# Optimization experiments

Hardware: AMD Instinct MI355X
Metric: run time of the kernel (lower is better)

The kernel has to match this reference:

```python
import jax, jax.numpy as jnp
import numpy as np


def setup_inputs() -> dict:
    key = jax.random.key(0)
    k1, k2, k3, k4 = jax.random.split(key, 4)
    B, T, M = 4, 2048, 1024   # batch, seq, d_model -> S = 8192 tokens
    E, F = 16, 4096           # experts (world_size*num_local_experts), d_ff
    x = jax.random.normal(k1, (B, T, M), dtype=jnp.float32) * 0.02
    Wg = jax.random.normal(k2, (M, E), dtype=jnp.float32) * 0.02
    w1 = jax.random.normal(k3, (E, M, F), dtype=jnp.float32) * 0.02
    w2 = jax.random.normal(k4, (E, F, M), dtype=jnp.float32) * 0.02
    return {"x": x, "Wg": Wg, "w1": w1, "w2": w2}


def reference(x, Wg, w1, w2):
    d = x.shape[-1]
    xr = x.reshape(-1, d)                     # (S, M)
    S = xr.shape[0]
    E = Wg.shape[1]
    C = (S + E - 1) // E                      # capacity (capacity_factor = 1.0)

    # top-1 gating (gate module = linear + softmax)
    gate = jax.nn.softmax(xr @ Wg, axis=-1)   # (S, E)
    idx = jnp.argmax(gate, axis=1)            # (S,) expert index per token
    gates_s = jnp.take_along_axis(gate, idx[:, None], axis=1)[:, 0]  # (S,)

    # cumulative-sum location within chosen expert
    onehot = jax.nn.one_hot(idx, E, dtype=jnp.int32)           # (S, E)
    loc = jnp.sum((jnp.cumsum(onehot, axis=0) - 1) * onehot, axis=1)  # (S,)
    valid = loc < C                                             # capacity drop mask

    # scatter dispatch: overflow tokens routed to a pad slot C, then sliced off
    loc_pad = jnp.minimum(loc, C)
    dispatched = jnp.zeros((E, C + 1, d), dtype=x.dtype).at[idx, loc_pad].set(xr)
    dispatched = dispatched[:, :C]            # (E, C, M)

    # all-to-all is identity (FakeAllToAllOp); per-expert FFN
    h = jax.nn.relu(jnp.einsum('ecm,emf->ecf', dispatched, w1))   # (E, C, F)
    expert_out = jnp.einsum('ecf,efm->ecm', h, w2)                # (E, C, M)

    # gather combine: rout[i] = gate_s[i] * expert_out[idx[i], loc[i]] if loc < C
    gathered = expert_out[idx, jnp.minimum(loc, C - 1)]           # (S, M)
    combined = gathered * (gates_s * valid.astype(x.dtype))[:, None]
    return combined.reshape(x.shape)
```

## Files before the change

kernel.cpp:

```cpp
#include <hip/hip_runtime.h>
#include <cstdint>
#include <cstddef>

#define S_TOK 8192
#define DM    1024
#define NE    16
#define NF    4096
#define CAP   512

typedef __attribute__((ext_vector_type(8))) short bf16x8;
typedef __attribute__((ext_vector_type(4))) float f32x4;

__device__ __forceinline__ unsigned short f2bf(float f) {
  __bf16 b = (__bf16)f;
  return __builtin_bit_cast(unsigned short, b);
}
__device__ __forceinline__ unsigned pk2(float a, float b) {
  return (unsigned)f2bf(a) | ((unsigned)f2bf(b) << 16);
}
__device__ __forceinline__ int pcol(int c) { return c ^ ((c >> 3) & 7); }

__device__ __forceinline__ void gload_lds16(const void* g, void* l) {
  __builtin_amdgcn_global_load_lds(
      (const __attribute__((address_space(1))) void*)g,
      (__attribute__((address_space(3))) void*)l, 16, 0, 0);
}

__global__ void __launch_bounds__(256)
cvt_kernel(const float* __restrict__ X, unsigned short* __restrict__ Xb) {
  const int t = blockIdx.x * 256 + threadIdx.x;
  const float4* src = (const float4*)X + (size_t)t * 4;
  float4 v0 = src[0], v1 = src[1], v2 = src[2], v3 = src[3];
  uint4 o0 = make_uint4(pk2(v0.x, v0.y), pk2(v0.z, v0.w),
                        pk2(v1.x, v1.y), pk2(v1.z, v1.w));
  uint4 o1 = make_uint4(pk2(v2.x, v2.y), pk2(v2.z, v2.w),
                        pk2(v3.x, v3.y), pk2(v3.z, v3.w));
  uint4* dst = (uint4*)Xb + (size_t)t * 2;
  dst[0] = o0; dst[1] = o1;
}

__global__ void __launch_bounds__(256)
gate_kernel(const float* __restrict__ X, const float* __restrict__ Wg,
            int* __restrict__ idx, float* __restrict__ gval) {
  const int tid  = threadIdx.x;
  const int lane = tid & 63;
  const int wid  = tid >> 6;
  const int e = lane & 15, q = lane >> 4;
  const int t0 = blockIdx.x * 16 + wid * 4;
  const int mbase = q * 256;

  const float* xp0 = X + (size_t)(t0 + 0) * DM + mbase;
  const float* xp1 = X + (size_t)(t0 + 1) * DM + mbase;
  const float* xp2 = X + (size_t)(t0 + 2) * DM + mbase;
  const float* xp3 = X + (size_t)(t0 + 3) * DM + mbase;
  const float* wp  = Wg + (size_t)mbase * NE + e;

  float a0 = 0.f, a1 = 0.f, a2 = 0.f, a3 = 0.f;
#pragma unroll 4
  for (int i = 0; i < 64; ++i) {
    float4 x0 = *(const float4*)(xp0 + i * 4);
    float4 x1 = *(const float4*)(xp1 + i * 4);
    float4 x2 = *(const float4*)(xp2 + i * 4);
    float4 x3 = *(const float4*)(xp3 + i * 4);
    float w0 = wp[(i * 4 + 0) * NE];
    float w1 = wp[(i * 4 + 1) * NE];
    float w2 = wp[(i * 4 + 2) * NE];
    float w3 = wp[(i * 4 + 3) * NE];
    a0 = fmaf(x0.x, w0, fmaf(x0.y, w1, fmaf(x0.z, w2, fmaf(x0.w, w3, a0))));
    a1 = fmaf(x1.x, w0, fmaf(x1.y, w1, fmaf(x1.z, w2, fmaf(x1.w, w3, a1))));
    a2 = fmaf(x2.x, w0, fmaf(x2.y, w1, fmaf(x2.z, w2, fmaf(x2.w, w3, a2))));
    a3 = fmaf(x3.x, w0, fmaf(x3.y, w1, fmaf(x3.z, w2, fmaf(x3.w, w3, a3))));
  }
#pragma unroll
  for (int s = 16; s < 64; s <<= 1) {
    a0 += __shfl_xor(a0, s, 64);
    a1 += __shfl_xor(a1, s, 64);
    a2 += __shfl_xor(a2, s, 64);
    a3 += __shfl_xor(a3, s, 64);
  }
  float l = (q == 0) ? a0 : (q == 1) ? a1 : (q == 2) ? a2 : a3;
  float bv = l; int bi = e;
#pragma unroll
  for (int s = 1; s < 16; s <<= 1) {
    float ov = __shfl_xor(bv, s, 16);
    int   oi = __shfl_xor(bi, s, 16);
    if (ov > bv || (ov == bv && oi < bi)) { bv = ov; bi = oi; }
  }
  float p  = expf(l - bv);
  float sm = p;
#pragma unroll
  for (int s = 1; s < 16; s <<= 1) sm += __shfl_xor(sm, s, 16);
  if (e == 0) {
    idx[t0 + q]  = bi;
    gval[t0 + q] = 1.0f / sm;
  }
}

__global__ void __launch_bounds__(1024)
scan_kernel(const int* __restrict__ idx, int* __restrict__ s2t) {
  const int tid = threadIdx.x;
#pragma unroll
  for (int k = 0; k < 8; ++k) s2t[tid + k * 1024] = -1;
  __shared__ int base[16];
  __shared__ int wavecnt[16][16];
  if (tid < 16) base[tid] = 0;
  __syncthreads();
  const int wid = tid >> 6, lane = tid & 63;
  const unsigned long long ltmask = (1ull << lane) - 1ull;
  for (int c = 0; c < 8; ++c) {
    const int t = c * 1024 + tid;
    const int e = idx[t];
    int rank = 0;
#pragma unroll
    for (int ee = 0; ee < 16; ++ee) {
      unsigned long long m = __ballot(e == ee);
      if (lane == 0) wavecnt[wid][ee] = __popcll(m);
      if (ee == e) rank = __popcll(m & ltmask);
    }
    __syncthreads();
    if (tid < 16) {
      int s = base[tid];
#pragma unroll
      for (int w = 0; w < 16; ++w) { int cc = wavecnt[w][tid]; wavecnt[w][tid] = s; s += cc; }
      base[tid] = s;
    }
    __syncthreads();
    const int loc = wavecnt[wid][e] + rank;
    if (loc < CAP) s2t[e * CAP + loc] = t;
    __syncthreads();
  }
}



#define G1_BX 2
#define G1_BY 32
#define G1_BZ 16
__global__ void __launch_bounds__(512, 2)
gemm1_kernel(const unsigned short* __restrict__ Xb, const float* __restrict__ W1,
             const int* __restrict__ s2t, unsigned short* __restrict__ H2) {
  constexpr int NT = DM / 64;
  __shared__ __align__(16) char lds[131072];

  const int tid = threadIdx.x;
  const int lane = tid & 63, wid = tid >> 6;
  const int wr = wid >> 1, wc = wid & 1;
  const int ln15 = lane & 15, l16 = lane >> 4;

  int flat = blockIdx.x + G1_BX * (blockIdx.y + G1_BY * blockIdx.z);
  flat = (flat & 7) * (G1_BX * G1_BY * G1_BZ / 8) + (flat >> 3);
  const int bx = flat % G1_BX;
  const int by = (flat / G1_BX) % G1_BY;
  const int e  = flat / (G1_BX * G1_BY);
  const int m0 = bx * 256, n0 = by * 128;

  char* const Bb0 = lds + 98304;
  char* const Bb1 = lds + 98304 + 16384;

  const int rb = wid >> 1;
  const int tok = s2t[e * CAP + m0 + rb * 64 + lane];
  const char* const asrc = (const char*)Xb + (size_t)(tok < 0 ? 0 : tok) * 2048;
  const int kgw = (wid & 1) * 4;
  const int adst = kgw * 4096 + rb * 1024;

  const int c0 = (tid & 31) * 4;
  const int kq = tid >> 5;
  const float* const bsrc = W1 + (size_t)e * DM * NF + (size_t)(kq * 4) * NF + n0 + c0;
  const int kgb = kq >> 1, hb = kq & 1;
  int bwoff[4];
#pragma unroll
  for (int cc = 0; cc < 4; ++cc) bwoff[cc] = kgb * 2048 + pcol(c0 + cc) * 16 + hb * 8;

  int aoff[4], boff[4];
#pragma unroll
  for (int mi = 0; mi < 4; ++mi) aoff[mi] = l16 * 4096 + (wr * 64 + mi * 16 + ln15) * 16;
#pragma unroll
  for (int ni = 0; ni < 4; ++ni) boff[ni] = l16 * 2048 + pcol(wc * 64 + ni * 16 + ln15) * 16;

  f32x4 acc[4][4];
#pragma unroll
  for (int mi = 0; mi < 4; ++mi)
#pragma unroll
    for (int ni = 0; ni < 4; ++ni) acc[mi][ni] = f32x4{0.f, 0.f, 0.f, 0.f};

  float4 breg[4];

  auto ISSUE_B = [&](int kt) {
    const float* bp = bsrc + (size_t)kt * 64 * NF;
#pragma unroll
    for (int r = 0; r < 4; ++r) breg[r] = *(const float4*)(bp + (size_t)r * NF);
  };
  auto ISSUE_A = [&](int Aoff, int kt) {
#pragma unroll
    for (int j = 0; j < 4; ++j)
      gload_lds16(asrc + kt * 128 + (kgw + j) * 16, lds + Aoff + adst + j * 4096);
  };
  auto WRITEB = [&](char* Bbuf) {
    const float* f = (const float*)breg;
#pragma unroll
    for (int cc = 0; cc < 4; ++cc)
      *(uint2*)(Bbuf + bwoff[cc]) =
          make_uint2(pk2(f[0 + cc], f[4 + cc]), pk2(f[8 + cc], f[12 + cc]));
  };
  auto COMPUTE = [&](int Aoff, const char* Bbuf) {
#pragma unroll
    for (int kk = 0; kk < 2; ++kk) {
      bf16x8 af[4], bf[4];
#pragma unroll
      for (int mi = 0; mi < 4; ++mi)
        af[mi] = *(const bf16x8*)(lds + Aoff + kk * 16384 + aoff[mi]);
#pragma unroll
      for (int ni = 0; ni < 4; ++ni)
        bf[ni] = *(const bf16x8*)(Bbuf + kk * 8192 + boff[ni]);
#pragma unroll
      for (int mi = 0; mi < 4; ++mi)
#pragma unroll
        for (int ni = 0; ni < 4; ++ni)
          acc[mi][ni] = __builtin_amdgcn_mfma_f32_16x16x32_bf16(af[mi], bf[ni], acc[mi][ni], 0, 0, 0);
    }
  };

  ISSUE_B(0); ISSUE_A(0, 0);
  WRITEB(Bb0);
  ISSUE_B(1); ISSUE_A(32768, 1);
  asm volatile("s_waitcnt vmcnt(8) lgkmcnt(0)" ::: "memory");
  __builtin_amdgcn_s_barrier();

  int aCur = 0, aNxt = 32768, aNx2 = 65536;
  for (int kt = 0; kt < NT; ++kt) {
    WRITEB((kt & 1) ? Bb0 : Bb1);
    const int tl = (kt + 2 < NT) ? kt + 2 : NT - 1;
    ISSUE_B(tl);
    ISSUE_A(aNx2, tl);
    COMPUTE(aCur, (kt & 1) ? Bb1 : Bb0);
    asm volatile("s_waitcnt vmcnt(8) lgkmcnt(0)" ::: "memory");
    __builtin_amdgcn_s_barrier();
    const int t = aCur; aCur = aNxt; aNxt = aNx2; aNx2 = t;
  }
  asm volatile("s_waitcnt vmcnt(0)" ::: "memory");
  __builtin_amdgcn_s_barrier();

  char* img = lds;
#pragma unroll
  for (int mi = 0; mi < 4; ++mi) {
#pragma unroll
    for (int ni = 0; ni < 4; ++ni) {
      const int colL = wc * 64 + ni * 16 + ln15;
      const int basei = (colL >> 6) * 32768 + ((colL >> 3) & 7) * 4096 + (colL & 7) * 2;
#pragma unroll
      for (int j = 0; j < 4; ++j) {
        const int rowL = wr * 64 + mi * 16 + l16 * 4 + j;
        float v = acc[mi][ni][j];
        v = v > 0.f ? v : 0.f;
        *(unsigned short*)(img + basei + rowL * 16) = f2bf(v);
      }
    }
  }
  __syncthreads();
  const char* src = img + tid * 128;
  char* dst = (char*)H2 + (size_t)e * 4194304 +
              (size_t)((n0 >> 6) + (tid >> 8)) * 65536 +
              (size_t)((tid >> 5) & 7) * 8192 +
              (size_t)(m0 + (tid & 31) * 8) * 16;
#pragma unroll
  for (int u = 0; u < 8; ++u)
    *(uint4*)(dst + u * 16) = *(const uint4*)(src + u * 16);
}

#define G2_BX 2
#define G2_BY 8
#define G2_BZ 16
__global__ void __launch_bounds__(512, 2)
gemm2_kernel(const unsigned short* __restrict__ H2, const float* __restrict__ W2,
             const int* __restrict__ s2t, const float* __restrict__ gval,
             float* __restrict__ Out) {
  constexpr int NT = NF / 64;
  __shared__ __align__(16) char lds[131072];

  const int tid = threadIdx.x;
  const int lane = tid & 63, wid = tid >> 6;
  const int wr = wid >> 1, wc = wid & 1;
  const int ln15 = lane & 15, l16 = lane >> 4;

  int flat = blockIdx.x + G2_BX * (blockIdx.y + G2_BY * blockIdx.z);
  flat = (flat & 7) * (G2_BX * G2_BY * G2_BZ / 8) + (flat >> 3);
  const int bx = flat % G2_BX;
  const int by = (flat / G2_BX) % G2_BY;
  const int e  = flat / (G2_BX * G2_BY);
  const int m0 = bx * 256, n0 = by * 128;

  char* const Bb0 = lds + 98304;
  char* const Bb1 = lds + 98304 + 16384;

  const int rb = wid >> 1;
  const int kgw = (wid & 1) * 4;
  const int adst = kgw * 4096 + rb * 1024;
  const char* const Hex = (const char*)H2 + (size_t)e * 4194304 + (size_t)m0 * 16 +
                          (size_t)(rb * 64 + lane) * 16;

  const int c0 = (tid & 31) * 4;
  const int kq = tid >> 5;
  const float* const bsrc = W2 + (size_t)e * NF * DM + (size_t)(kq * 4) * DM + n0 + c0;
  const int kgb = kq >> 1, hb = kq & 1;
  int bwoff[4];
#pragma unroll
  for (int cc = 0; cc < 4; ++cc) bwoff[cc] = kgb * 2048 + pcol(c0 + cc) * 16 + hb * 8;

  int aoff[4], boff[4];
#pragma unroll
  for (int mi = 0; mi < 4; ++mi) aoff[mi] = l16 * 4096 + (wr * 64 + mi * 16 + ln15) * 16;
#pragma unroll
  for (int ni = 0; ni < 4; ++ni) boff[ni] = l16 * 2048 + pcol(wc * 64 + ni * 16 + ln15) * 16;

  f32x4 acc[4][4];
#pragma unroll
  for (int mi = 0; mi < 4; ++mi)
#pragma unroll
    for (int ni = 0; ni < 4; ++ni) acc[mi][ni] = f32x4{0.f, 0.f, 0.f, 0.f};

  float4 breg[4];

  auto ISSUE_B = [&](int kt) {
    const float* bp = bsrc + (size_t)kt * 64 * DM;
#pragma unroll
    for (int r = 0; r < 4; ++r) breg[r] = *(const float4*)(bp + (size_t)r * DM);
  };
  auto ISSUE_A = [&](int Aoff, int kt) {
#pragma unroll
    for (int j = 0; j < 4; ++j)
      gload_lds16(Hex + (size_t)kt * 65536 + (size_t)(kgw + j) * 8192,
                  lds + Aoff + adst + j * 4096);
  };
  auto WRITEB = [&](char* Bbuf) {
    const float* f = (const float*)breg;
#pragma unroll
    for (int cc = 0; cc < 4; ++cc)
      *(uint2*)(Bbuf + bwoff[cc]) =
          make_uint2(pk2(f[0 + cc], f[4 + cc]), pk2(f[8 + cc], f[12 + cc]));
  };
  auto COMPUTE = [&](int Aoff, const char* Bbuf) {
#pragma unroll
    for (int kk = 0; kk < 2; ++kk) {
      bf16x8 af[4], bf[4];
#pragma unroll
      for (int mi = 0; mi < 4; ++mi)
        af[mi] = *(const bf16x8*)(lds + Aoff + kk * 16384 + aoff[mi]);
#pragma unroll
      for (int ni = 0; ni < 4; ++ni)
        bf[ni] = *(const bf16x8*)(Bbuf + kk * 8192 + boff[ni]);
#pragma unroll
      for (int mi = 0; mi < 4; ++mi)
#pragma unroll
        for (int ni = 0; ni < 4; ++ni)
          acc[mi][ni] = __builtin_amdgcn_mfma_f32_16x16x32_bf16(af[mi], bf[ni], acc[mi][ni], 0, 0, 0);
    }
  };

  ISSUE_B(0); ISSUE_A(0, 0);
  WRITEB(Bb0);
  ISSUE_B(1); ISSUE_A(32768, 1);
  asm volatile("s_waitcnt vmcnt(8) lgkmcnt(0)" ::: "memory");
  __builtin_amdgcn_s_barrier();

  int aCur = 0, aNxt = 32768, aNx2 = 65536;
  for (int kt = 0; kt < NT; ++kt) {
    WRITEB((kt & 1) ? Bb0 : Bb1);
    const int tl = (kt + 2 < NT) ? kt + 2 : NT - 1;
    ISSUE_B(tl);
    ISSUE_A(aNx2, tl);
    COMPUTE(aCur, (kt & 1) ? Bb1 : Bb0);
    asm volatile("s_waitcnt vmcnt(8) lgkmcnt(0)" ::: "memory");
    __builtin_amdgcn_s_barrier();
    const int t = aCur; aCur = aNxt; aNxt = aNx2; aNx2 = t;
  }
  asm volatile("s_waitcnt vmcnt(0)" ::: "memory");

#pragma unroll
  for (int mi = 0; mi < 4; ++mi) {
#pragma unroll
    for (int ni = 0; ni < 4; ++ni) {
      const int col = n0 + wc * 64 + ni * 16 + ln15;
#pragma unroll
      for (int j = 0; j < 4; ++j) {
        const int row = m0 + wr * 64 + mi * 16 + l16 * 4 + j;
        const int tk = s2t[e * CAP + row];
        if (tk >= 0)
          Out[(size_t)tk * DM + col] = acc[mi][ni][j] * gval[tk];
      }
    }
  }
}

extern "C" void kernel_launch(void* const* d_in, const int* in_sizes, int n_in,
                              void* d_out, int out_size, void* d_ws, size_t ws_size,
                              hipStream_t stream) {
  (void)in_sizes; (void)n_in; (void)ws_size;
  const float* X  = (const float*)d_in[0];
  const float* Wg = (const float*)d_in[1];
  const float* W1 = (const float*)d_in[2];
  const float* W2 = (const float*)d_in[3];
  float* Out = (float*)d_out;

  char* ws = (char*)d_ws;
  int*   s2t  = (int*)ws;
  int*   idx  = (int*)(ws + 32768);
  float* gval = (float*)(ws + 65536);
  unsigned short* Xb = (unsigned short*)(ws + 98304);
  unsigned short* H2 = (unsigned short*)(ws + 98304 + 16777216);

  (void)hipMemsetAsync(d_out, 0, (size_t)out_size * sizeof(float), stream);
  cvt_kernel<<<2048, 256, 0, stream>>>(X, Xb);
  gate_kernel<<<S_TOK / 16, 256, 0, stream>>>(X, Wg, idx, gval);
  scan_kernel<<<1, 1024, 0, stream>>>(idx, s2t);
  gemm1_kernel<<<dim3(G1_BX, G1_BY, G1_BZ), 512, 0, stream>>>(Xb, W1, s2t, H2);
  gemm2_kernel<<<dim3(G2_BX, G2_BY, G2_BZ), 512, 0, stream>>>(H2, W2, s2t, gval, Out);
}
```

Measured before the change: 305.2 us.

## Replace bf16 convert with gather into k-major dispatched layout; remap XCD blocks

Drops the whole-tensor bf16 conversion and instead gathers only the dispatched tokens after the scan, converting to bf16 and writing them in a k-group-major per-expert layout. gemm1 then loads A tiles with contiguous, coalesced 16-byte loads and no longer does a per-lane token indirection. Block-to-expert mapping is also changed so each XCD handles two whole experts, aiming for better L2 reuse of expert weights. The gather now runs after the scan on the critical path instead of in parallel with gating, and it zero-fills empty slots.

Measured after the change: 280.7 us. 1.09x faster.

```diff
diff --git a/kernel.cpp b/kernel.cpp
--- a/kernel.cpp
+++ b/kernel.cpp
@@ -24,19 +24,6 @@
   __builtin_amdgcn_global_load_lds(
       (const __attribute__((address_space(1))) void*)g,
       (__attribute__((address_space(3))) void*)l, 16, 0, 0);
-}
-
-__global__ void __launch_bounds__(256)
-cvt_kernel(const float* __restrict__ X, unsigned short* __restrict__ Xb) {
-  const int t = blockIdx.x * 256 + threadIdx.x;
-  const float4* src = (const float4*)X + (size_t)t * 4;
-  float4 v0 = src[0], v1 = src[1], v2 = src[2], v3 = src[3];
-  uint4 o0 = make_uint4(pk2(v0.x, v0.y), pk2(v0.z, v0.w),
-                        pk2(v1.x, v1.y), pk2(v1.z, v1.w));
-  uint4 o1 = make_uint4(pk2(v2.x, v2.y), pk2(v2.z, v2.w),
-                        pk2(v3.x, v3.y), pk2(v3.z, v3.w));
-  uint4* dst = (uint4*)Xb + (size_t)t * 2;
-  dst[0] = o0; dst[1] = o1;
 }
 
 __global__ void __launch_bounds__(256)
@@ -131,14 +118,42 @@
   }
 }
 
+__global__ void __launch_bounds__(256)
+gather_kernel(const float* __restrict__ X, const int* __restrict__ s2t,
+              unsigned short* __restrict__ Xg) {
+  const int tid = threadIdx.x;
+  const int d  = tid & 127;
+  const int sl = tid >> 7;
+  const int s0 = blockIdx.x * 16;
+#pragma unroll 2
+  for (int p = 0; p < 8; ++p) {
+    const int s = s0 + p * 2 + sl;
+    const int tok = s2t[s];
+    uint4 w;
+    if (tok >= 0) {
+      const float* xp = X + (size_t)tok * DM + d * 8;
+      float4 v0 = *(const float4*)xp;
+      float4 v1 = *(const float4*)(xp + 4);
+      w = make_uint4(pk2(v0.x, v0.y), pk2(v0.z, v0.w),
+                     pk2(v1.x, v1.y), pk2(v1.z, v1.w));
+    } else {
+      w = make_uint4(0u, 0u, 0u, 0u);
+    }
+    char* dst = (char*)Xg + (size_t)(s >> 9) * 1048576 +
+                (size_t)(d >> 3) * 65536 + (size_t)(d & 7) * 8192 +
+                (size_t)(s & 511) * 16;
+    *(uint4*)dst = w;
+  }
+}
+
 
 
 #define G1_BX 2
 #define G1_BY 32
 #define G1_BZ 16
 __global__ void __launch_bounds__(512, 2)
-gemm1_kernel(const unsigned short* __restrict__ Xb, const float* __restrict__ W1,
-             const int* __restrict__ s2t, unsigned short* __restrict__ H2) {
+gemm1_kernel(const unsigned short* __restrict__ Xg, const float* __restrict__ W1,
+             unsigned short* __restrict__ H2) {
   constexpr int NT = DM / 64;
   __shared__ __align__(16) char lds[131072];
 
@@ -147,21 +162,21 @@
   const int wr = wid >> 1, wc = wid & 1;
   const int ln15 = lane & 15, l16 = lane >> 4;
 
-  int flat = blockIdx.x + G1_BX * (blockIdx.y + G1_BY * blockIdx.z);
-  flat = (flat & 7) * (G1_BX * G1_BY * G1_BZ / 8) + (flat >> 3);
-  const int bx = flat % G1_BX;
-  const int by = (flat / G1_BX) % G1_BY;
-  const int e  = flat / (G1_BX * G1_BY);
+  const int flat = blockIdx.x + G1_BX * (blockIdx.y + G1_BY * blockIdx.z);
+  const int xcd = flat & 7, jj = flat >> 3;
+  const int e  = xcd * 2 + (jj >> 6);
+  const int rr = jj & 63;
+  const int by = rr >> 1, bx = rr & 1;
   const int m0 = bx * 256, n0 = by * 128;
 
   char* const Bb0 = lds + 98304;
   char* const Bb1 = lds + 98304 + 16384;
 
   const int rb = wid >> 1;
-  const int tok = s2t[e * CAP + m0 + rb * 64 + lane];
-  const char* const asrc = (const char*)Xb + (size_t)(tok < 0 ? 0 : tok) * 2048;
   const int kgw = (wid & 1) * 4;
   const int adst = kgw * 4096 + rb * 1024;
+  const char* const Xge = (const char*)Xg + (size_t)e * 1048576 +
+                          (size_t)(m0 + rb * 64 + lane) * 16;
 
   const int c0 = (tid & 31) * 4;
   const int kq = tid >> 5;
@@ -193,7 +208,8 @@
   auto ISSUE_A = [&](int Aoff, int kt) {
 #pragma unroll
     for (int j = 0; j < 4; ++j)
-      gload_lds16(asrc + kt * 128 + (kgw + j) * 16, lds + Aoff + adst + j * 4096);
+      gload_lds16(Xge + (size_t)kt * 65536 + (size_t)(kgw + j) * 8192,
+                  lds + Aoff + adst + j * 4096);
   };
   auto WRITEB = [&](char* Bbuf) {
     const float* f = (const float*)breg;
@@ -282,11 +298,11 @@
   const int wr = wid >> 1, wc = wid & 1;
   const int ln15 = lane & 15, l16 = lane >> 4;
 
-  int flat = blockIdx.x + G2_BX * (blockIdx.y + G2_BY * blockIdx.z);
-  flat = (flat & 7) * (G2_BX * G2_BY * G2_BZ / 8) + (flat >> 3);
-  const int bx = flat % G2_BX;
-  const int by = (flat / G2_BX) % G2_BY;
-  const int e  = flat / (G2_BX * G2_BY);
+  const int flat = blockIdx.x + G2_BX * (blockIdx.y + G2_BY * blockIdx.z);
+  const int xcd = flat & 7, jj = flat >> 3;
+  const int e  = xcd * 2 + (jj >> 4);
+  const int rr = jj & 15;
+  const int by = rr >> 1, bx = rr & 1;
   const int m0 = bx * 256, n0 = by * 128;
 
   char* const Bb0 = lds + 98304;
@@ -405,13 +421,13 @@
   int*   s2t  = (int*)ws;
   int*   idx  = (int*)(ws + 32768);
   float* gval = (float*)(ws + 65536);
-  unsigned short* Xb = (unsigned short*)(ws + 98304);
+  unsigned short* Xg = (unsigned short*)(ws + 98304);
   unsigned short* H2 = (unsigned short*)(ws + 98304 + 16777216);
 
   (void)hipMemsetAsync(d_out, 0, (size_t)out_size * sizeof(float), stream);
-  cvt_kernel<<<2048, 256, 0, stream>>>(X, Xb);
   gate_kernel<<<S_TOK / 16, 256, 0, stream>>>(X, Wg, idx, gval);
   scan_kernel<<<1, 1024, 0, stream>>>(idx, s2t);
-  gemm1_kernel<<<dim3(G1_BX, G1_BY, G1_BZ), 512, 0, stream>>>(Xb, W1, s2t, H2);
+  gather_kernel<<<512, 256, 0, stream>>>(X, s2t, Xg);
+  gemm1_kernel<<<dim3(G1_BX, G1_BY, G1_BZ), 512, 0, stream>>>(Xg, W1, H2);
   gemm2_kernel<<<dim3(G2_BX, G2_BY, G2_BZ), 512, 0, stream>>>(H2, W2, s2t, gval, Out);
 }
```
